# Kernel tuning notes

Hardware: AMD Instinct MI355X
Metric: run time of the kernel (lower is better)

## Reference

```python
import jax, jax.numpy as jnp
import numpy as np

B, A, E = 1024, 256, 4      # batch, PBC atoms per sample, num element types
M1, M2 = 128, 16            # descriptor dims
H1, H2 = 32, 64             # embedding-net hidden sizes


def setup_inputs() -> dict:
    key = jax.random.key(0)
    ks = jax.random.split(key, 9)
    # Packed sample layout: [s (2A interleaved value,type), R_tilde (4A), N_i]
    vals = jax.random.normal(ks[0], (B, A), dtype=jnp.float32)
    types = jax.random.randint(ks[1], (B, A), 0, E).astype(jnp.float32)
    s = jnp.stack([vals, types], axis=-1).reshape(B, 2 * A)
    R = jax.random.normal(ks[2], (B, 4 * A), dtype=jnp.float32)
    n_col = jnp.full((B, 1), float(A), dtype=jnp.float32)  # all atoms valid
    x = jnp.concatenate([s, R, n_col], axis=1)  # [B, 6A+1]
    # Per-element-type MLP params, stacked over the expert (element) axis
    W1 = jax.random.normal(ks[3], (E, 1, H1), dtype=jnp.float32)
    b1 = jax.random.normal(ks[4], (E, H1), dtype=jnp.float32) * 0.1
    W2 = jax.random.normal(ks[5], (E, H1, H2), dtype=jnp.float32) / np.sqrt(H1)
    b2 = jax.random.normal(ks[6], (E, H2), dtype=jnp.float32) * 0.1
    W3 = jax.random.normal(ks[7], (E, H2, M1), dtype=jnp.float32) / np.sqrt(H2)
    b3 = jax.random.normal(ks[8], (E, M1), dtype=jnp.float32) * 0.1
    return {"x": x, "W1": W1, "b1": b1, "W2": W2, "b2": b2, "W3": W3, "b3": b3}


def reference(x, W1, b1, W2, b2, W3, b3):
    Bsz = x.shape[0]
    Apad = (x.shape[1] - 1) // 6  # PBC_atom_num
    s = x[:, : 2 * Apad].reshape(Bsz, Apad, 2)       # [B,A,2] (value, type)
    R = x[:, 2 * Apad : 6 * Apad].reshape(Bsz, Apad, 4)  # [B,A,4]
    N = x[:, -1].astype(jnp.int32)                   # valid atoms per sample
    mask = (jnp.arange(Apad)[None, :] < N[:, None]).astype(x.dtype)  # [B,A]

    v = s[..., 0:1]                                   # [B,A,1] scalar MLP input
    t = jnp.clip(s[..., 1].astype(jnp.int32), 0, W1.shape[0] - 1)  # [B,A]

    # Run every expert MLP on all atoms, then gather by element type.
    h = jax.nn.relu(jnp.einsum('bai,eio->ebao', v, W1) + b1[:, None, None, :])
    h = jax.nn.relu(jnp.einsum('ebai,eio->ebao', h, W2) + b2[:, None, None, :])
    g_all = jnp.einsum('ebai,eio->ebao', h, W3) + b3[:, None, None, :]  # [E,B,A,M1]
    g = jnp.take_along_axis(jnp.moveaxis(g_all, 0, 2), t[:, :, None, None], axis=2)[:, :, 0]  # [B,A,M1]

    g = g * mask[..., None]  # zero out padded atoms (rows beyond N_i)
    g2 = g[..., :M2]

    # D_i = g^T R R^T g2, batched
    P = jnp.einsum('bam,bac->bmc', g, R)    # [B,M1,4]
    Q = jnp.einsum('bac,bam->bcm', R, g2)   # [B,4,M2]
    D = jnp.einsum('bmc,bcn->bmn', P, Q)    # [B,M1,M2]
    return D.reshape(Bsz, -1)
```

## Files before the change

### kernel.cpp

```cpp
#include <hip/hip_runtime.h>

#define XROW 1537
#define NTHR 256
#define SP   320


__device__ __forceinline__ float rlf(float x, int u) {
    return __uint_as_float(__builtin_amdgcn_readlane(__float_as_uint(x), u));
}
__device__ __forceinline__ int rli(int x, int u) {
    return __builtin_amdgcn_readlane(x, u);
}

__global__ void __launch_bounds__(256)
be_prep(const float* __restrict__ W1, const float* __restrict__ b1,
        const float* __restrict__ W2, const float* __restrict__ b2,
        float* __restrict__ ws)
{
    __shared__ float t_s[4][32], w1_s[4][32], b1_s[4][32];
    __shared__ int   rnk[4][32];
    __shared__ float ACd[4][33][128];
    const int tid = threadIdx.x;
    const int w = tid >> 6, lane = tid & 63;
    const int e = w;

    if (lane < 32) {
        float w1v = W1[e * 32 + lane], b1v = b1[e * 32 + lane];
        w1_s[e][lane] = w1v;
        b1_s[e][lane] = b1v;
        t_s[e][lane] = (w1v != 0.f) ? (-b1v / w1v) : 3.4e38f;
    }
    for (int idx = tid; idx < 4 * 33 * 128; idx += 256)
        (&ACd[0][0][0])[idx] = 0.f;
    __syncthreads();
    if (lane < 32) {
        float ti = t_s[e][lane];
        int rank = 0;
        for (int j = 0; j < 32; ++j) {
            float tj = t_s[e][j];
            rank += (tj < ti) || (tj == ti && j < lane);
        }
        rnk[e][lane] = rank;
        ws[e * 32 + rank] = ti;
    }
    __syncthreads();

    const int o = lane;
    float A = 0.f, C = b2[e * 64 + o];
    #pragma unroll
    for (int i = 0; i < 32; ++i) {
        float w1v = w1_s[e][i], b1v = b1_s[e][i];
        float w2v = W2[(e * 32 + i) * 64 + o];
        if ((w1v < 0.f) || (w1v == 0.f && b1v > 0.f)) {
            A = fmaf(w1v, w2v, A);
            C = fmaf(b1v, w2v, C);
        }
        if (w1v != 0.f) {
            int r = rnk[e][i];
            float s = (w1v > 0.f) ? 1.f : -1.f;
            ACd[e][r + 1][2 * o]     = s * w1v * w2v;
            ACd[e][r + 1][2 * o + 1] = s * b1v * w2v;
        }
    }
    float* AC = ws + 128;
    float2 p; p.x = A; p.y = C;
    *(float2*)&AC[(e * 33 + 0) * 128 + 2 * o] = p;
    for (int k = 1; k <= 32; ++k) {
        A += ACd[e][k][2 * o];
        C += ACd[e][k][2 * o + 1];
        p.x = A; p.y = C;
        *(float2*)&AC[(e * 33 + k) * 128 + 2 * o] = p;
    }
}

__global__ void __launch_bounds__(NTHR)
be_kernel(const float* __restrict__ x,
          const float* __restrict__ W3, const float* __restrict__ b3,
          const float* __restrict__ wsr,
          float* __restrict__ out)
{
    __shared__ int2   kv[SP];
    __shared__ __align__(16) float4 Rm4[SP];
    __shared__ float Ts_l[128];
    __shared__ __align__(16) float Spart[4][4][64][4];
    __shared__ __align__(16) float Sred[4][64][4];
    __shared__ __align__(16) float Pp[4][128][4];
    __shared__ float Pr5[128 * 5];
    __shared__ float Tpart[4][4][16];
    __shared__ float T16[16];
    __shared__ int   cntw[4][4];

    const int tid  = threadIdx.x;
    const int b    = blockIdx.x;
    const int lane = tid & 63;
    const int w    = tid >> 6;
    const long xb  = (long)b * XROW;
    const float* ACg = wsr + 128;

    float v = x[xb + 2 * tid];
    int e = (int)x[xb + 2 * tid + 1];
    e = max(0, min(3, e));
    int N = (int)x[xb + 1536];
    float maskf = (tid < N) ? 1.f : 0.f;
    if (tid < 128) Ts_l[tid] = wsr[tid];

    unsigned long long mybal = 0ull;
    #pragma unroll
    for (int q = 0; q < 4; ++q) {
        unsigned long long bq = __ballot(e == q);
        if (lane == 0) cntw[w][q] = __popcll(bq);
        if (e == q) mybal = bq;
    }
    int rank = __popcll(mybal & ((1ull << lane) - 1ull));

    for (int idx = tid; idx < SP; idx += NTHR) {
        kv[idx] = make_int2(0, 0);
        Rm4[idx] = make_float4(0.f, 0.f, 0.f, 0.f);
    }
    __syncthreads();

    int c0 = cntw[0][0] + cntw[1][0] + cntw[2][0] + cntw[3][0];
    int c1 = cntw[0][1] + cntw[1][1] + cntw[2][1] + cntw[3][1];
    int c2_ = cntw[0][2] + cntw[1][2] + cntw[2][2] + cntw[3][2];
    int c3 = cntw[0][3] + cntw[1][3] + cntw[2][3] + cntw[3][3];
    const int B0 = 0;
    const int B1 = (B0 + c0 + 3) & ~3;
    const int B2 = (B1 + c1 + 3) & ~3;
    const int B3 = (B2 + c2_ + 3) & ~3;
    const int St4 = (B3 + c3 + 3) & ~3;

    {
        int offw = 0;
        #pragma unroll
        for (int w2 = 0; w2 < 4; ++w2) if (w2 < w) offw += cntw[w2][e];
        int Bsel = (e == 0) ? B0 : ((e == 1) ? B1 : ((e == 2) ? B2 : B3));
        int ci = Bsel + offw + rank;
        kv[ci] = make_int2(0, __float_as_int(v));
        float4 r4;
        r4.x = x[xb + 512 + 4 * tid + 0] * maskf;
        r4.y = x[xb + 512 + 4 * tid + 1] * maskf;
        r4.z = x[xb + 512 + 4 * tid + 2] * maskf;
        r4.w = x[xb + 512 + 4 * tid + 3] * maskf;
        Rm4[ci] = r4;
    }
    __syncthreads();

    for (int a2 = tid; a2 < St4; a2 += NTHR) {
        int ev = (a2 >= B1) + (a2 >= B2) + (a2 >= B3);
        float va = __int_as_float(kv[a2].y);
        const float* Ts = &Ts_l[ev * 32];
        int k = 0;
        #pragma unroll
        for (int st = 32; st >= 1; st >>= 1)
            if (k + st <= 32 && Ts[k + st - 1] <= va) k += st;
        kv[a2].x = (ev * 33 + k) * 128;
    }

    {
        int te = tid >> 6, tc = (tid >> 4) & 3, tk = tid & 15;
        int s0 = (te == 0) ? B0 : ((te == 1) ? B1 : ((te == 2) ? B2 : B3));
        int s1 = (te == 0) ? B1 : ((te == 1) ? B2 : ((te == 2) ? B3 : St4));
        float ts = 0.f;
        for (int s = s0 + tk; s < s1; s += 16) ts += ((const float*)&Rm4[s])[tc];
        Tpart[te][tc][tk] = ts;
    }
    __syncthreads();
    if (tid < 16) {
        float t = 0.f;
        #pragma unroll
        for (int k = 0; k < 16; ++k) t += Tpart[tid >> 2][tid & 3][k];
        T16[tid] = t;
    }

    float Se[4][4];
    #pragma unroll
    for (int i = 0; i < 4; ++i)
        #pragma unroll
        for (int j = 0; j < 4; ++j) Se[i][j] = 0.f;

    #pragma unroll
    for (int t = 0; t < 5; ++t) {
        const int base = t * 64 + w * 16;
        int2   kvu = kv[base + (lane & 15)];
        float4 r4u = Rm4[base + (lane & 15)];

        float2 ac16[16];
        #pragma unroll
        for (int u = 0; u < 16; ++u) {
            int s_k = rli(kvu.x, u);
            ac16[u] = *(const float2*)&ACg[s_k + 2 * lane];
        }
        #pragma unroll
        for (int g = 0; g < 4; ++g) {
            float t0 = 0.f, t1 = 0.f, t2 = 0.f, t3 = 0.f;
            #pragma unroll
            for (int u4 = 0; u4 < 4; ++u4) {
                const int u = g * 4 + u4;
                float s_v = rlf(__int_as_float(kvu.y), u);
                float h = fmaxf(fmaf(s_v, ac16[u].x, ac16[u].y), 0.f);
                t0 = fmaf(h, rlf(r4u.x, u), t0);
                t1 = fmaf(h, rlf(r4u.y, u), t1);
                t2 = fmaf(h, rlf(r4u.z, u), t2);
                t3 = fmaf(h, rlf(r4u.w, u), t3);
            }
            const int gb = base + g * 4;
            const int eg = (gb >= B1) + (gb >= B2) + (gb >= B3);
            #pragma unroll
            for (int ee = 0; ee < 4; ++ee) {
                float fe = (eg == ee) ? 1.f : 0.f;
                Se[ee][0] = fmaf(t0, fe, Se[ee][0]);
                Se[ee][1] = fmaf(t1, fe, Se[ee][1]);
                Se[ee][2] = fmaf(t2, fe, Se[ee][2]);
                Se[ee][3] = fmaf(t3, fe, Se[ee][3]);
            }
        }
    }
    #pragma unroll
    for (int ee = 0; ee < 4; ++ee) {
        float4 s4; s4.x = Se[ee][0]; s4.y = Se[ee][1];
                   s4.z = Se[ee][2]; s4.w = Se[ee][3];
        *(float4*)&Spart[w][ee][lane][0] = s4;
    }
    __syncthreads();

    {
        const int e_ = tid >> 6, i_ = tid & 63;
        float4 s0 = *(const float4*)&Spart[0][e_][i_][0];
        float4 s1 = *(const float4*)&Spart[1][e_][i_][0];
        float4 s2 = *(const float4*)&Spart[2][e_][i_][0];
        float4 s3 = *(const float4*)&Spart[3][e_][i_][0];
        float4 r; r.x = (s0.x + s1.x) + (s2.x + s3.x);
                  r.y = (s0.y + s1.y) + (s2.y + s3.y);
                  r.z = (s0.z + s1.z) + (s2.z + s3.z);
                  r.w = (s0.w + s1.w) + (s2.w + s3.w);
        *(float4*)&Sred[e_][i_][0] = r;
    }
    __syncthreads();

    {
        float a0 = 0.f, a1 = 0.f, a2 = 0.f, a3 = 0.f;
        float b0 = 0.f, b1_ = 0.f, b2_ = 0.f, b3_ = 0.f;
        const float* W3e = W3 + w * 8192;
        #pragma unroll 8
        for (int i = 0; i < 64; ++i) {
            const float4 s4 = *(const float4*)&Sred[w][i][0];
            float wa = W3e[i * 128 + lane];
            float wb = W3e[i * 128 + 64 + lane];
            a0 = fmaf(wa, s4.x, a0); a1 = fmaf(wa, s4.y, a1);
            a2 = fmaf(wa, s4.z, a2); a3 = fmaf(wa, s4.w, a3);
            b0 = fmaf(wb, s4.x, b0); b1_ = fmaf(wb, s4.y, b1_);
            b2_ = fmaf(wb, s4.z, b2_); b3_ = fmaf(wb, s4.w, b3_);
        }
        const float4 t4 = *(const float4*)&T16[w * 4];
        float bya = b3[w * 128 + lane];
        float byb = b3[w * 128 + 64 + lane];
        a0 = fmaf(bya, t4.x, a0); a1 = fmaf(bya, t4.y, a1);
        a2 = fmaf(bya, t4.z, a2); a3 = fmaf(bya, t4.w, a3);
        b0 = fmaf(byb, t4.x, b0); b1_ = fmaf(byb, t4.y, b1_);
        b2_ = fmaf(byb, t4.z, b2_); b3_ = fmaf(byb, t4.w, b3_);
        float4 pa; pa.x = a0; pa.y = a1; pa.z = a2; pa.w = a3;
        float4 pb; pb.x = b0; pb.y = b1_; pb.z = b2_; pb.w = b3_;
        *(float4*)&Pp[w][lane][0]      = pa;
        *(float4*)&Pp[w][lane + 64][0] = pb;
    }
    __syncthreads();

    {
        const int m = tid >> 1, cp = tid & 1;
        float2 p0 = *(const float2*)&Pp[0][m][2 * cp];
        float2 p1 = *(const float2*)&Pp[1][m][2 * cp];
        float2 p2 = *(const float2*)&Pp[2][m][2 * cp];
        float2 p3 = *(const float2*)&Pp[3][m][2 * cp];
        Pr5[m * 5 + 2 * cp]     = (p0.x + p1.x) + (p2.x + p3.x);
        Pr5[m * 5 + 2 * cp + 1] = (p0.y + p1.y) + (p2.y + p3.y);
    }
    __syncthreads();

    {
        const int m   = tid >> 1;
        const int nb8 = (tid & 1) << 3;
        float pm0 = Pr5[m * 5 + 0], pm1 = Pr5[m * 5 + 1];
        float pm2 = Pr5[m * 5 + 2], pm3 = Pr5[m * 5 + 3];
        float o8[8];
        #pragma unroll
        for (int r = 0; r < 8; ++r) {
            int n = nb8 + r;
            float d = pm0 * Pr5[n * 5 + 0];
            d = fmaf(pm1, Pr5[n * 5 + 1], d);
            d = fmaf(pm2, Pr5[n * 5 + 2], d);
            d = fmaf(pm3, Pr5[n * 5 + 3], d);
            o8[r] = d;
        }
        float* outb = out + (long)b * 2048 + tid * 8;
        float4 s0; s0.x = o8[0]; s0.y = o8[1]; s0.z = o8[2]; s0.w = o8[3];
        float4 s1; s1.x = o8[4]; s1.y = o8[5]; s1.z = o8[6]; s1.w = o8[7];
        *(float4*)&outb[0] = s0;
        *(float4*)&outb[4] = s1;
    }
}

extern "C" void kernel_launch(void* const* d_in, const int* in_sizes, int n_in,
                              void* d_out, int out_size, void* d_ws, size_t ws_size,
                              hipStream_t stream)
{
    const float* x  = (const float*)d_in[0];
    const float* W1 = (const float*)d_in[1];
    const float* b1 = (const float*)d_in[2];
    const float* W2 = (const float*)d_in[3];
    const float* b2 = (const float*)d_in[4];
    const float* W3 = (const float*)d_in[5];
    const float* b3 = (const float*)d_in[6];
    float* out = (float*)d_out;
    float* ws  = (float*)d_ws;

    be_prep<<<1, 256, 0, stream>>>(W1, b1, W2, b2, ws);
    be_kernel<<<1024, NTHR, 0, stream>>>(x, W3, b3, ws, out);
}
```

Measured before the change: 37.76 us.

## Parallelize be_prep across 132 blocks, one per expert and breakpoint segment

The prep kernel ran as a single block: it built a shared-memory delta table and walked a sequential 33-step prefix sum per expert. It now launches 132 one-wave blocks, one per (expert, segment). Each block recomputes the ranks with readlane and evaluates the active-unit mask for its own segment directly, which removes the LDS table, the barriers and the serial scan. The cost is 33x redundant rank computation and W2 reads, and summing directly per segment can round slightly differently from the old prefix sum.

After: 32.46 us. -14.0%, faster.

```diff
diff --git a/kernel.cpp b/kernel.cpp
--- a/kernel.cpp
+++ b/kernel.cpp
@@ -12,65 +12,46 @@
     return __builtin_amdgcn_readlane(x, u);
 }
 
-__global__ void __launch_bounds__(256)
+__global__ void __launch_bounds__(64)
 be_prep(const float* __restrict__ W1, const float* __restrict__ b1,
         const float* __restrict__ W2, const float* __restrict__ b2,
         float* __restrict__ ws)
 {
-    __shared__ float t_s[4][32], w1_s[4][32], b1_s[4][32];
-    __shared__ int   rnk[4][32];
-    __shared__ float ACd[4][33][128];
-    const int tid = threadIdx.x;
-    const int w = tid >> 6, lane = tid & 63;
-    const int e = w;
-
+    const int e    = blockIdx.x / 33;
+    const int k    = blockIdx.x % 33;
+    const int lane = threadIdx.x;
+
+    float w1v_l = 0.f, b1v_l = 0.f, ti = 3.4e38f;
     if (lane < 32) {
-        float w1v = W1[e * 32 + lane], b1v = b1[e * 32 + lane];
-        w1_s[e][lane] = w1v;
-        b1_s[e][lane] = b1v;
-        t_s[e][lane] = (w1v != 0.f) ? (-b1v / w1v) : 3.4e38f;
-    }
-    for (int idx = tid; idx < 4 * 33 * 128; idx += 256)
-        (&ACd[0][0][0])[idx] = 0.f;
-    __syncthreads();
-    if (lane < 32) {
-        float ti = t_s[e][lane];
-        int rank = 0;
-        for (int j = 0; j < 32; ++j) {
-            float tj = t_s[e][j];
-            rank += (tj < ti) || (tj == ti && j < lane);
-        }
-        rnk[e][lane] = rank;
-        ws[e * 32 + rank] = ti;
-    }
-    __syncthreads();
+        w1v_l = W1[e * 32 + lane];
+        b1v_l = b1[e * 32 + lane];
+        ti = (w1v_l != 0.f) ? (-b1v_l / w1v_l) : 3.4e38f;
+    }
+    int rank = 0;
+    #pragma unroll
+    for (int j = 0; j < 32; ++j) {
+        float tj = rlf(ti, j);
+        rank += (tj < ti) || (tj == ti && j < lane);
+    }
+    if (k == 0 && lane < 32) ws[e * 32 + rank] = ti;
 
     const int o = lane;
     float A = 0.f, C = b2[e * 64 + o];
     #pragma unroll
     for (int i = 0; i < 32; ++i) {
-        float w1v = w1_s[e][i], b1v = b1_s[e][i];
+        float w1v = rlf(w1v_l, i);
+        float b1v = rlf(b1v_l, i);
+        int   r   = rli(rank, i);
         float w2v = W2[(e * 32 + i) * 64 + o];
-        if ((w1v < 0.f) || (w1v == 0.f && b1v > 0.f)) {
-            A = fmaf(w1v, w2v, A);
-            C = fmaf(b1v, w2v, C);
-        }
-        if (w1v != 0.f) {
-            int r = rnk[e][i];
-            float s = (w1v > 0.f) ? 1.f : -1.f;
-            ACd[e][r + 1][2 * o]     = s * w1v * w2v;
-            ACd[e][r + 1][2 * o + 1] = s * b1v * w2v;
-        }
+        bool act = (w1v > 0.f) ? (k > r)
+                 : ((w1v < 0.f) ? (k <= r) : (b1v > 0.f));
+        float m = act ? 1.f : 0.f;
+        A = fmaf(w1v * m, w2v, A);
+        C = fmaf(b1v * m, w2v, C);
     }
     float* AC = ws + 128;
     float2 p; p.x = A; p.y = C;
-    *(float2*)&AC[(e * 33 + 0) * 128 + 2 * o] = p;
-    for (int k = 1; k <= 32; ++k) {
-        A += ACd[e][k][2 * o];
-        C += ACd[e][k][2 * o + 1];
-        p.x = A; p.y = C;
-        *(float2*)&AC[(e * 33 + k) * 128 + 2 * o] = p;
-    }
+    *(float2*)&AC[(e * 33 + k) * 128 + 2 * o] = p;
 }
 
 __global__ void __launch_bounds__(NTHR)
@@ -313,6 +294,6 @@
     float* out = (float*)d_out;
     float* ws  = (float*)d_ws;
 
-    be_prep<<<1, 256, 0, stream>>>(W1, b1, W2, b2, ws);
+    be_prep<<<132, 64, 0, stream>>>(W1, b1, W2, b2, ws);
     be_kernel<<<1024, NTHR, 0, stream>>>(x, W3, b3, ws, out);
 }
```
